# Kernel tuning notes

Hardware: AMD Instinct MI355X
Metric: run time of the kernel (lower is better)

## Reference

```python
import jax, jax.numpy as jnp
import numpy as np

DIM, HEADS, WH, WW, MLAT, MLON = 512, 8, 8, 8, 32, 64
N = WH * WW
B = MLAT * MLON
PER_LAT = (2 * WH - 1) * (2 * WW - 1)  # 225


def _make_rel_idx():
    # Swin 2D relative position index inside one window
    ch, cw = np.arange(WH), np.arange(WW)
    coords = np.stack(np.meshgrid(ch, cw, indexing='ij')).reshape(2, -1)  # (2, N)
    rel = coords[:, :, None] - coords[:, None, :]                          # (2, N, N)
    rel = rel.transpose(1, 2, 0).astype(np.int64)
    rel[..., 0] += WH - 1
    rel[..., 1] += WW - 1
    rel[..., 0] *= 2 * WW - 1
    idx2d = rel.sum(-1)                                                    # (N, N)
    # earth-specific: each lat row i gets its own 225-entry slab; lon diff is 0
    idx = idx2d[None] + np.arange(MLAT)[:, None, None] * PER_LAT           # (Mlat, N, N)
    idx = np.broadcast_to(idx[:, None], (MLAT, MLON, N, N)).reshape(B, N, N)
    return jnp.asarray(idx.astype(np.int32))


def setup_inputs() -> dict:
    key = jax.random.key(0)
    k = jax.random.split(key, 5)
    x = jax.random.normal(k[0], (B, N, DIM), dtype=jnp.float32)
    w_qkv = jax.random.normal(k[1], (3 * DIM, DIM), dtype=jnp.float32) * 0.02
    b_qkv = jnp.zeros((3 * DIM,), dtype=jnp.float32)
    w_proj = jax.random.normal(k[2], (DIM, DIM), dtype=jnp.float32) * 0.02
    b_proj = jnp.zeros((DIM,), dtype=jnp.float32)
    bias_table = jax.random.normal(k[3], (MLAT * PER_LAT, HEADS), dtype=jnp.float32) * 0.02
    return {
        'x': x, 'w_qkv': w_qkv, 'b_qkv': b_qkv,
        'w_proj': w_proj, 'b_proj': b_proj,
        'bias_table': bias_table, 'rel_idx': _make_rel_idx(),
    }


def reference(x, w_qkv, b_qkv, w_proj, b_proj, bias_table, rel_idx):
    Bn, Nn, C = x.shape
    D = C // HEADS
    qkv = (x @ w_qkv.T + b_qkv).reshape(Bn, Nn, 3, HEADS, D)
    q = jnp.transpose(qkv[:, :, 0], (0, 2, 1, 3))  # (B, H, N, D)
    k = jnp.transpose(qkv[:, :, 1], (0, 2, 1, 3))
    v = jnp.transpose(qkv[:, :, 2], (0, 2, 1, 3))
    # gather learned earth bias: (B, N, N, H) -> (B, H, N, N)
    bias = jnp.transpose(bias_table[rel_idx], (0, 3, 1, 2))
    scale = D ** -0.5  # SDPA default scale (qk_scale is None)
    attn = jax.nn.softmax(jnp.einsum('bhnd,bhmd->bhnm', q, k) * scale + bias, axis=-1)
    out = jnp.einsum('bhnm,bhmd->bhnd', attn, v)
    out = jnp.transpose(out, (0, 2, 1, 3)).reshape(Bn, Nn, C)
    return out @ w_proj.T + b_proj
```

## Files before the change

### kernel.cpp

```cpp
#include <hip/hip_runtime.h>
#include <stdint.h>

typedef __attribute__((ext_vector_type(8))) short short8;
typedef __attribute__((ext_vector_type(4))) short short4v;
typedef __attribute__((ext_vector_type(4))) float float4v;

__device__ __forceinline__ short f2bf(float f) {
  uint32_t u = __builtin_bit_cast(uint32_t, f);
  u += 0x7FFFu + ((u >> 16) & 1u);
  return (short)(u >> 16);
}

__device__ __forceinline__ void gl_lds16(const short* g, short* l) {
  __builtin_amdgcn_global_load_lds(
      (const __attribute__((address_space(1))) unsigned int*)g,
      (__attribute__((address_space(3))) unsigned int*)l, 16, 0, 0);
}


__global__ void prep_weights(const float* __restrict__ wq, const float* __restrict__ wp,
                             short* __restrict__ wq_b, short* __restrict__ wp_b) {
  int i = blockIdx.x * blockDim.x + threadIdx.x;
  int stride = gridDim.x * blockDim.x;
  for (int j = i; j < 786432 / 4; j += stride) {
    float4 v = ((const float4*)wq)[j];
    short4v t = {f2bf(v.x), f2bf(v.y), f2bf(v.z), f2bf(v.w)};
    ((short4v*)wq_b)[j] = t;
  }
  for (int j = i; j < 262144 / 4; j += stride) {
    float4 v = ((const float4*)wp)[j];
    short4v t = {f2bf(v.x), f2bf(v.y), f2bf(v.z), f2bf(v.w)};
    ((short4v*)wp_b)[j] = t;
  }
}

__global__ __launch_bounds__(1024, 4)
void qkv_attn(const float* __restrict__ x, const short* __restrict__ wq,
              const float* __restrict__ bqkv, const float* __restrict__ btab,
              short* __restrict__ attn) {
  __shared__ short Xs[64 * 512];
  __shared__ short Qs[4][64 * 64];
  __shared__ short Ks[4][64 * 64];
  __shared__ short Vt[4][64 * 64];

  const int b    = blockIdx.x;
  const int tid  = threadIdx.x;
  const int lane = tid & 63;
  const int w    = tid >> 6;
  const int l16  = lane & 15;
  const int quad = lane >> 4;
  const int lat  = b >> 6;
  const int r    = l16 & 7;
  const int offE = ((quad ^ (r & 3)) << 3) | ((r >> 2) << 5);
  const int offO = offE ^ 32;

  const float* xw = x + (size_t)b * (64 * 512);
  for (int c = tid; c < 64 * 128; c += 1024) {
    int n = c >> 7, kc = c & 127;
    float4 v = *(const float4*)(xw + n * 512 + kc * 4);
    short4v t = {f2bf(v.x), f2bf(v.y), f2bf(v.z), f2bf(v.w)};
    *(short4v*)&Xs[n * 512 + ((kc * 4) ^ ((n & 7) << 3))] = t;
  }
  __syncthreads();

  const int g  = w >> 2;
  const int st = w & 3;

#pragma unroll 1
  for (int h0 = 0; h0 < 8; h0 += 4) {
    {
      const int hq = h0 + g;
      const int hk = h0 + (g ^ 1);
      const short* Aq = wq + (size_t)((hq * 64 + st * 16 + l16) * 512) + quad * 8;
      const short* Ak = wq + (size_t)((512 + hk * 64 + st * 16 + l16) * 512) + quad * 8;
      const short* Av = wq + (size_t)((1024 + hq * 64 + st * 16 + l16) * 512) + quad * 8;
      const short* xE = &Xs[l16 * 512 + offE];
      const short* xO = &Xs[l16 * 512 + offO];

      float4v aQ[4] = {}, aK[4] = {}, aV[4] = {};
#pragma unroll
      for (int j = 0; j < 16; ++j) {
        const short* xb = (j & 1) ? xO : xE;
        const int xoff = (j >> 1) * 64;
        short8 wqf = *(const short8*)(Aq + j * 32);
        short8 wkf = *(const short8*)(Ak + j * 32);
        short8 wvf = *(const short8*)(Av + j * 32);
        short8 x0 = *(const short8*)(xb + xoff);
        short8 x1 = *(const short8*)(xb + 8192 + xoff);
        short8 x2 = *(const short8*)(xb + 16384 + xoff);
        short8 x3 = *(const short8*)(xb + 24576 + xoff);
        aQ[0] = __builtin_amdgcn_mfma_f32_16x16x32_bf16(wqf, x0, aQ[0], 0, 0, 0);
        aQ[1] = __builtin_amdgcn_mfma_f32_16x16x32_bf16(wqf, x1, aQ[1], 0, 0, 0);
        aQ[2] = __builtin_amdgcn_mfma_f32_16x16x32_bf16(wqf, x2, aQ[2], 0, 0, 0);
        aQ[3] = __builtin_amdgcn_mfma_f32_16x16x32_bf16(wqf, x3, aQ[3], 0, 0, 0);
        aK[0] = __builtin_amdgcn_mfma_f32_16x16x32_bf16(wkf, x0, aK[0], 0, 0, 0);
        aK[1] = __builtin_amdgcn_mfma_f32_16x16x32_bf16(wkf, x1, aK[1], 0, 0, 0);
        aK[2] = __builtin_amdgcn_mfma_f32_16x16x32_bf16(wkf, x2, aK[2], 0, 0, 0);
        aK[3] = __builtin_amdgcn_mfma_f32_16x16x32_bf16(wkf, x3, aK[3], 0, 0, 0);
        aV[0] = __builtin_amdgcn_mfma_f32_16x16x32_bf16(x0, wvf, aV[0], 0, 0, 0);
        aV[1] = __builtin_amdgcn_mfma_f32_16x16x32_bf16(x1, wvf, aV[1], 0, 0, 0);
        aV[2] = __builtin_amdgcn_mfma_f32_16x16x32_bf16(x2, wvf, aV[2], 0, 0, 0);
        aV[3] = __builtin_amdgcn_mfma_f32_16x16x32_bf16(x3, wvf, aV[3], 0, 0, 0);
      }

      float bq[4], bk[4];
#pragma unroll
      for (int i = 0; i < 4; ++i) {
        bq[i] = bqkv[hq * 64 + st * 16 + quad * 4 + i];
        bk[i] = bqkv[512 + hk * 64 + st * 16 + quad * 4 + i];
      }
      short* dq = &Qs[g][0];
      short* dk = &Ks[g ^ 1][0];
      const int swqk = (st * 16 + quad * 4) ^ (r << 3);
#pragma unroll
      for (int t = 0; t < 4; ++t) {
        int n = t * 16 + l16;
        short4v pq, pk;
#pragma unroll
        for (int i = 0; i < 4; ++i) {
          pq[i] = f2bf((aQ[t][i] + bq[i]) * 0.125f);
          pk[i] = f2bf(aK[t][i] + bk[i]);
        }
        *(short4v*)&dq[n * 64 + swqk] = pq;
        *(short4v*)&dk[n * 64 + swqk] = pk;
      }
      float bv = bqkv[1024 + hq * 64 + st * 16 + l16];
      const int dv = st * 16 + l16;
#pragma unroll
      for (int t = 0; t < 4; ++t) {
        short4v pv;
#pragma unroll
        for (int i = 0; i < 4; ++i) pv[i] = f2bf(aV[t][i] + bv);
        *(short4v*)&Vt[g][dv * 64 + ((t * 16 + quad * 4) ^ (r << 3))] = pv;
      }
    }
    __syncthreads();

    {
      const int hsel = w >> 2;
      const int h    = h0 + hsel;
      const int n0   = (w & 3) * 16;
      const short* Qb = &Qs[hsel][0];
      const short* Kb = &Ks[hsel][0];
      const short* Vb = &Vt[hsel][0];

      float4v s4[4] = {};
#pragma unroll
      for (int j = 0; j < 2; ++j) {
        const int o = j ? offO : offE;
        short8 a = *(const short8*)&Qb[(n0 + l16) * 64 + o];
#pragma unroll
        for (int t = 0; t < 4; ++t) {
          short8 bf = *(const short8*)&Kb[(t * 16 + l16) * 64 + o];
          s4[t] = __builtin_amdgcn_mfma_f32_16x16x32_bf16(a, bf, s4[t], 0, 0, 0);
        }
      }
#pragma unroll
      for (int t = 0; t < 4; ++t) {
        int m = t * 16 + l16;
#pragma unroll
        for (int i = 0; i < 4; ++i) {
          int n = n0 + quad * 4 + i;
          int idx = ((n >> 3) - (m >> 3) + 7) * 15 + ((n & 7) - (m & 7) + 7) + lat * 225;
          s4[t][i] += btab[idx * 8 + h];
        }
      }
      float p[4][4];
#pragma unroll
      for (int i = 0; i < 4; ++i) {
        float mx = fmaxf(fmaxf(s4[0][i], s4[1][i]), fmaxf(s4[2][i], s4[3][i]));
        mx = fmaxf(mx, __shfl_xor(mx, 1));
        mx = fmaxf(mx, __shfl_xor(mx, 2));
        mx = fmaxf(mx, __shfl_xor(mx, 4));
        mx = fmaxf(mx, __shfl_xor(mx, 8));
        float e0 = __expf(s4[0][i] - mx), e1 = __expf(s4[1][i] - mx);
        float e2 = __expf(s4[2][i] - mx), e3 = __expf(s4[3][i] - mx);
        float sm = e0 + e1 + e2 + e3;
        sm += __shfl_xor(sm, 1);
        sm += __shfl_xor(sm, 2);
        sm += __shfl_xor(sm, 4);
        sm += __shfl_xor(sm, 8);
        float inv = 1.0f / sm;
        p[0][i] = e0 * inv; p[1][i] = e1 * inv; p[2][i] = e2 * inv; p[3][i] = e3 * inv;
      }
      short* Pw = &Qs[hsel][0];
#pragma unroll
      for (int t = 0; t < 4; ++t)
#pragma unroll
        for (int i = 0; i < 4; ++i) {
          int row = n0 + quad * 4 + i;
          Pw[row * 64 + ((t * 16 + l16) ^ ((row & 7) << 3))] = f2bf(p[t][i]);
        }

      float4v o4[4] = {};
#pragma unroll
      for (int j = 0; j < 2; ++j) {
        const int o = j ? offO : offE;
        short8 a = *(const short8*)&Qb[(n0 + l16) * 64 + o];
#pragma unroll
        for (int t = 0; t < 4; ++t) {
          short8 bf = *(const short8*)&Vb[(t * 16 + l16) * 64 + o];
          o4[t] = __builtin_amdgcn_mfma_f32_16x16x32_bf16(a, bf, o4[t], 0, 0, 0);
        }
      }
      short* ob = attn + (size_t)b * (64 * 512);
#pragma unroll
      for (int t = 0; t < 4; ++t)
#pragma unroll
        for (int i = 0; i < 4; ++i)
          ob[(n0 + quad * 4 + i) * 512 + h * 64 + t * 16 + l16] = f2bf(o4[t][i]);
    }
    __syncthreads();
  }
}

__device__ __forceinline__ void stage_tile(const short* __restrict__ ga,
                                           const short* __restrict__ gb,
                                           short* lA, short* lB,
                                           int w, int srow, int scol) {
#pragma unroll
  for (int j = 0; j < 2; ++j) {
    int c = w * 2 + j;
    gl_lds16(ga + (size_t)(c * 8 + srow) * 512 + scol, &lA[c * 512]);
    gl_lds16(gb + (size_t)(c * 8 + srow) * 512 + scol, &lB[c * 512]);
  }
}

__device__ __forceinline__ void compute_tile(const short* As_, const short* Bs_,
                                             float4v (&acc)[2][4],
                                             int wm, int wn, int l16,
                                             int offE, int offO) {
#pragma unroll
  for (int ks = 0; ks < 2; ++ks) {
    const int o = ks ? offO : offE;
    short8 a[2], bf[4];
#pragma unroll
    for (int ti = 0; ti < 2; ++ti)
      a[ti] = *(const short8*)&As_[(wm * 32 + ti * 16 + l16) * 64 + o];
#pragma unroll
    for (int tj = 0; tj < 4; ++tj)
      bf[tj] = *(const short8*)&Bs_[(wn * 64 + tj * 16 + l16) * 64 + o];
#pragma unroll
    for (int ti = 0; ti < 2; ++ti)
#pragma unroll
      for (int tj = 0; tj < 4; ++tj)
        acc[ti][tj] = __builtin_amdgcn_mfma_f32_16x16x32_bf16(a[ti], bf[tj], acc[ti][tj], 0, 0, 0);
  }
}

__global__ __launch_bounds__(512, 4)
void proj_gemm(const short* __restrict__ attn, const short* __restrict__ wp,
               const float* __restrict__ bproj, float* __restrict__ out) {
  __shared__ short As0[128 * 64];
  __shared__ short As1[128 * 64];
  __shared__ short Bs0[128 * 64];
  __shared__ short Bs1[128 * 64];

  const int orig = blockIdx.x;
  const int wg   = (orig & 7) * 512 + (orig >> 3);
  const int n0   = (wg & 3) * 128;
  const int m0   = (wg >> 2) * 128;

  const int tid  = threadIdx.x;
  const int lane = tid & 63;
  const int w    = tid >> 6;
  const int l16  = lane & 15;
  const int quad = lane >> 4;
  const int wm   = w >> 1, wn = w & 1;
  const int r    = l16 & 7;
  const int offE = ((quad ^ (r & 3)) << 3) | ((r >> 2) << 5);
  const int offO = offE ^ 32;

  const int srow = lane >> 3;
  const int scol = ((lane & 7) ^ srow) * 8;

  const short* gA = attn + (size_t)m0 * 512;
  const short* gB = wp + (size_t)n0 * 512;

  float4v acc[2][4] = {};

  stage_tile(gA, gB, As0, Bs0, w, srow, scol);
  __syncthreads();
#pragma unroll
  for (int kt = 0; kt < 8; kt += 2) {
    if (kt + 1 < 8) stage_tile(gA + (kt + 1) * 64, gB + (kt + 1) * 64, As1, Bs1, w, srow, scol);
    compute_tile(As0, Bs0, acc, wm, wn, l16, offE, offO);
    __syncthreads();
    if (kt + 2 < 8) stage_tile(gA + (kt + 2) * 64, gB + (kt + 2) * 64, As0, Bs0, w, srow, scol);
    compute_tile(As1, Bs1, acc, wm, wn, l16, offE, offO);
    __syncthreads();
  }

  float bj[4];
#pragma unroll
  for (int tj = 0; tj < 4; ++tj) bj[tj] = bproj[n0 + wn * 64 + tj * 16 + l16];
#pragma unroll
  for (int ti = 0; ti < 2; ++ti)
#pragma unroll
    for (int i = 0; i < 4; ++i) {
      size_t rowoff = (size_t)(m0 + wm * 32 + ti * 16 + quad * 4 + i) * 512;
#pragma unroll
      for (int tj = 0; tj < 4; ++tj)
        out[rowoff + n0 + wn * 64 + tj * 16 + l16] = acc[ti][tj][i] + bj[tj];
    }
}

extern "C" void kernel_launch(void* const* d_in, const int* in_sizes, int n_in,
                              void* d_out, int out_size, void* d_ws, size_t ws_size,
                              hipStream_t stream) {
  const float* x     = (const float*)d_in[0];
  const float* wqkv  = (const float*)d_in[1];
  const float* bqkv  = (const float*)d_in[2];
  const float* wproj = (const float*)d_in[3];
  const float* bproj = (const float*)d_in[4];
  const float* btab  = (const float*)d_in[5];
  float* out = (float*)d_out;

  short* wq_b = (short*)d_ws;
  short* wp_b = wq_b + 786432;
  short* attn = wp_b + 262144;

  prep_weights<<<256, 256, 0, stream>>>(wqkv, wproj, wq_b, wp_b);
  qkv_attn<<<2048, 1024, 0, stream>>>(x, wq_b, bqkv, btab, attn);
  proj_gemm<<<4096, 512, 0, stream>>>(attn, wp_b, bproj, out);
}
```

Before: 1.069 ms.

## Make attention and projection kernels persistent over multiple windows with weight prefetch

The fused QKV-attention kernel now processes four windows per block (512 blocks instead of 2048), and the projection GEMM processes four M tiles per block (1024 blocks instead of 4096). Bias loads are hoisted out of the GEMM tile loop. The QKV weight fragments are software-pipelined through a three-deep register ring so global loads are issued two steps ahead of the MFMAs. The intent is to cut block launch and prologue overhead and hide weight-load latency. The cost is fewer blocks, which may underfill the GPU or leave a tail imbalance, plus a serial per-window X staging step with no overlap.

```diff
diff --git a/kernel.cpp b/kernel.cpp
--- a/kernel.cpp
+++ b/kernel.cpp
@@ -43,174 +43,187 @@
   __shared__ short Ks[4][64 * 64];
   __shared__ short Vt[4][64 * 64];
 
-  const int b    = blockIdx.x;
+  const int blk  = blockIdx.x;
   const int tid  = threadIdx.x;
   const int lane = tid & 63;
   const int w    = tid >> 6;
   const int l16  = lane & 15;
   const int quad = lane >> 4;
-  const int lat  = b >> 6;
   const int r    = l16 & 7;
   const int offE = ((quad ^ (r & 3)) << 3) | ((r >> 2) << 5);
   const int offO = offE ^ 32;
 
-  const float* xw = x + (size_t)b * (64 * 512);
-  for (int c = tid; c < 64 * 128; c += 1024) {
-    int n = c >> 7, kc = c & 127;
-    float4 v = *(const float4*)(xw + n * 512 + kc * 4);
-    short4v t = {f2bf(v.x), f2bf(v.y), f2bf(v.z), f2bf(v.w)};
-    *(short4v*)&Xs[n * 512 + ((kc * 4) ^ ((n & 7) << 3))] = t;
-  }
-  __syncthreads();
-
   const int g  = w >> 2;
   const int st = w & 3;
 
 #pragma unroll 1
-  for (int h0 = 0; h0 < 8; h0 += 4) {
-    {
-      const int hq = h0 + g;
-      const int hk = h0 + (g ^ 1);
-      const short* Aq = wq + (size_t)((hq * 64 + st * 16 + l16) * 512) + quad * 8;
-      const short* Ak = wq + (size_t)((512 + hk * 64 + st * 16 + l16) * 512) + quad * 8;
-      const short* Av = wq + (size_t)((1024 + hq * 64 + st * 16 + l16) * 512) + quad * 8;
-      const short* xE = &Xs[l16 * 512 + offE];
-      const short* xO = &Xs[l16 * 512 + offO];
-
-      float4v aQ[4] = {}, aK[4] = {}, aV[4] = {};
-#pragma unroll
-      for (int j = 0; j < 16; ++j) {
-        const short* xb = (j & 1) ? xO : xE;
-        const int xoff = (j >> 1) * 64;
-        short8 wqf = *(const short8*)(Aq + j * 32);
-        short8 wkf = *(const short8*)(Ak + j * 32);
-        short8 wvf = *(const short8*)(Av + j * 32);
-        short8 x0 = *(const short8*)(xb + xoff);
-        short8 x1 = *(const short8*)(xb + 8192 + xoff);
-        short8 x2 = *(const short8*)(xb + 16384 + xoff);
-        short8 x3 = *(const short8*)(xb + 24576 + xoff);
-        aQ[0] = __builtin_amdgcn_mfma_f32_16x16x32_bf16(wqf, x0, aQ[0], 0, 0, 0);
-        aQ[1] = __builtin_amdgcn_mfma_f32_16x16x32_bf16(wqf, x1, aQ[1], 0, 0, 0);
-        aQ[2] = __builtin_amdgcn_mfma_f32_16x16x32_bf16(wqf, x2, aQ[2], 0, 0, 0);
-        aQ[3] = __builtin_amdgcn_mfma_f32_16x16x32_bf16(wqf, x3, aQ[3], 0, 0, 0);
-        aK[0] = __builtin_amdgcn_mfma_f32_16x16x32_bf16(wkf, x0, aK[0], 0, 0, 0);
-        aK[1] = __builtin_amdgcn_mfma_f32_16x16x32_bf16(wkf, x1, aK[1], 0, 0, 0);
-        aK[2] = __builtin_amdgcn_mfma_f32_16x16x32_bf16(wkf, x2, aK[2], 0, 0, 0);
-        aK[3] = __builtin_amdgcn_mfma_f32_16x16x32_bf16(wkf, x3, aK[3], 0, 0, 0);
-        aV[0] = __builtin_amdgcn_mfma_f32_16x16x32_bf16(x0, wvf, aV[0], 0, 0, 0);
-        aV[1] = __builtin_amdgcn_mfma_f32_16x16x32_bf16(x1, wvf, aV[1], 0, 0, 0);
-        aV[2] = __builtin_amdgcn_mfma_f32_16x16x32_bf16(x2, wvf, aV[2], 0, 0, 0);
-        aV[3] = __builtin_amdgcn_mfma_f32_16x16x32_bf16(x3, wvf, aV[3], 0, 0, 0);
-      }
-
-      float bq[4], bk[4];
-#pragma unroll
-      for (int i = 0; i < 4; ++i) {
-        bq[i] = bqkv[hq * 64 + st * 16 + quad * 4 + i];
-        bk[i] = bqkv[512 + hk * 64 + st * 16 + quad * 4 + i];
-      }
-      short* dq = &Qs[g][0];
-      short* dk = &Ks[g ^ 1][0];
-      const int swqk = (st * 16 + quad * 4) ^ (r << 3);
-#pragma unroll
-      for (int t = 0; t < 4; ++t) {
-        int n = t * 16 + l16;
-        short4v pq, pk;
-#pragma unroll
-        for (int i = 0; i < 4; ++i) {
-          pq[i] = f2bf((aQ[t][i] + bq[i]) * 0.125f);
-          pk[i] = f2bf(aK[t][i] + bk[i]);
-        }
-        *(short4v*)&dq[n * 64 + swqk] = pq;
-        *(short4v*)&dk[n * 64 + swqk] = pk;
-      }
-      float bv = bqkv[1024 + hq * 64 + st * 16 + l16];
-      const int dv = st * 16 + l16;
-#pragma unroll
-      for (int t = 0; t < 4; ++t) {
-        short4v pv;
-#pragma unroll
-        for (int i = 0; i < 4; ++i) pv[i] = f2bf(aV[t][i] + bv);
-        *(short4v*)&Vt[g][dv * 64 + ((t * 16 + quad * 4) ^ (r << 3))] = pv;
-      }
+  for (int vi = 0; vi < 4; ++vi) {
+    const int b   = blk * 4 + vi;
+    const int lat = b >> 6;
+
+    const float* xw = x + (size_t)b * (64 * 512);
+    for (int c = tid; c < 64 * 128; c += 1024) {
+      int n = c >> 7, kc = c & 127;
+      float4 v = *(const float4*)(xw + n * 512 + kc * 4);
+      short4v t = {f2bf(v.x), f2bf(v.y), f2bf(v.z), f2bf(v.w)};
+      *(short4v*)&Xs[n * 512 + ((kc * 4) ^ ((n & 7) << 3))] = t;
     }
     __syncthreads();
 
-    {
-      const int hsel = w >> 2;
-      const int h    = h0 + hsel;
-      const int n0   = (w & 3) * 16;
-      const short* Qb = &Qs[hsel][0];
-      const short* Kb = &Ks[hsel][0];
-      const short* Vb = &Vt[hsel][0];
-
-      float4v s4[4] = {};
-#pragma unroll
-      for (int j = 0; j < 2; ++j) {
-        const int o = j ? offO : offE;
-        short8 a = *(const short8*)&Qb[(n0 + l16) * 64 + o];
+#pragma unroll 1
+    for (int h0 = 0; h0 < 8; h0 += 4) {
+      {
+        const int hq = h0 + g;
+        const int hk = h0 + (g ^ 1);
+        const short* Aq = wq + (size_t)((hq * 64 + st * 16 + l16) * 512) + quad * 8;
+        const short* Ak = wq + (size_t)((512 + hk * 64 + st * 16 + l16) * 512) + quad * 8;
+        const short* Av = wq + (size_t)((1024 + hq * 64 + st * 16 + l16) * 512) + quad * 8;
+        const short* xE = &Xs[l16 * 512 + offE];
+        const short* xO = &Xs[l16 * 512 + offO];
+
+        short8 wqp[3], wkp[3], wvp[3];
+        wqp[0] = *(const short8*)(Aq);      wqp[1] = *(const short8*)(Aq + 32);
+        wkp[0] = *(const short8*)(Ak);      wkp[1] = *(const short8*)(Ak + 32);
+        wvp[0] = *(const short8*)(Av);      wvp[1] = *(const short8*)(Av + 32);
+
+        float4v aQ[4] = {}, aK[4] = {}, aV[4] = {};
+#pragma unroll
+        for (int j = 0; j < 16; ++j) {
+          if (j + 2 < 16) {
+            wqp[(j + 2) % 3] = *(const short8*)(Aq + (j + 2) * 32);
+            wkp[(j + 2) % 3] = *(const short8*)(Ak + (j + 2) * 32);
+            wvp[(j + 2) % 3] = *(const short8*)(Av + (j + 2) * 32);
+          }
+          const short* xb = (j & 1) ? xO : xE;
+          const int xoff = (j >> 1) * 64;
+          short8 x0 = *(const short8*)(xb + xoff);
+          short8 x1 = *(const short8*)(xb + 8192 + xoff);
+          short8 x2 = *(const short8*)(xb + 16384 + xoff);
+          short8 x3 = *(const short8*)(xb + 24576 + xoff);
+          short8 Wq = wqp[j % 3], Wk = wkp[j % 3], Wv = wvp[j % 3];
+          aQ[0] = __builtin_amdgcn_mfma_f32_16x16x32_bf16(Wq, x0, aQ[0], 0, 0, 0);
+          aQ[1] = __builtin_amdgcn_mfma_f32_16x16x32_bf16(Wq, x1, aQ[1], 0, 0, 0);
+          aQ[2] = __builtin_amdgcn_mfma_f32_16x16x32_bf16(Wq, x2, aQ[2], 0, 0, 0);
+          aQ[3] = __builtin_amdgcn_mfma_f32_16x16x32_bf16(Wq, x3, aQ[3], 0, 0, 0);
+          aK[0] = __builtin_amdgcn_mfma_f32_16x16x32_bf16(Wk, x0, aK[0], 0, 0, 0);
+          aK[1] = __builtin_amdgcn_mfma_f32_16x16x32_bf16(Wk, x1, aK[1], 0, 0, 0);
+          aK[2] = __builtin_amdgcn_mfma_f32_16x16x32_bf16(Wk, x2, aK[2], 0, 0, 0);
+          aK[3] = __builtin_amdgcn_mfma_f32_16x16x32_bf16(Wk, x3, aK[3], 0, 0, 0);
+          aV[0] = __builtin_amdgcn_mfma_f32_16x16x32_bf16(x0, Wv, aV[0], 0, 0, 0);
+          aV[1] = __builtin_amdgcn_mfma_f32_16x16x32_bf16(x1, Wv, aV[1], 0, 0, 0);
+          aV[2] = __builtin_amdgcn_mfma_f32_16x16x32_bf16(x2, Wv, aV[2], 0, 0, 0);
+          aV[3] = __builtin_amdgcn_mfma_f32_16x16x32_bf16(x3, Wv, aV[3], 0, 0, 0);
+        }
+
+        float bq[4], bk[4];
+#pragma unroll
+        for (int i = 0; i < 4; ++i) {
+          bq[i] = bqkv[hq * 64 + st * 16 + quad * 4 + i];
+          bk[i] = bqkv[512 + hk * 64 + st * 16 + quad * 4 + i];
+        }
+        short* dq = &Qs[g][0];
+        short* dk = &Ks[g ^ 1][0];
+        const int swqk = (st * 16 + quad * 4) ^ (r << 3);
 #pragma unroll
         for (int t = 0; t < 4; ++t) {
-          short8 bf = *(const short8*)&Kb[(t * 16 + l16) * 64 + o];
-          s4[t] = __builtin_amdgcn_mfma_f32_16x16x32_bf16(a, bf, s4[t], 0, 0, 0);
+          int n = t * 16 + l16;
+          short4v pq, pk;
+#pragma unroll
+          for (int i = 0; i < 4; ++i) {
+            pq[i] = f2bf((aQ[t][i] + bq[i]) * 0.125f);
+            pk[i] = f2bf(aK[t][i] + bk[i]);
+          }
+          *(short4v*)&dq[n * 64 + swqk] = pq;
+          *(short4v*)&dk[n * 64 + swqk] = pk;
+        }
+        float bv = bqkv[1024 + hq * 64 + st * 16 + l16];
+        const int dv = st * 16 + l16;
+#pragma unroll
+        for (int t = 0; t < 4; ++t) {
+          short4v pv;
+#pragma unroll
+          for (int i = 0; i < 4; ++i) pv[i] = f2bf(aV[t][i] + bv);
+          *(short4v*)&Vt[g][dv * 64 + ((t * 16 + quad * 4) ^ (r << 3))] = pv;
         }
       }
-#pragma unroll
-      for (int t = 0; t < 4; ++t) {
-        int m = t * 16 + l16;
+      __syncthreads();
+
+      {
+        const int hsel = w >> 2;
+        const int h    = h0 + hsel;
+        const int n0   = (w & 3) * 16;
+        const short* Qb = &Qs[hsel][0];
+        const short* Kb = &Ks[hsel][0];
+        const short* Vb = &Vt[hsel][0];
+
+        float4v s4[4] = {};
+#pragma unroll
+        for (int j = 0; j < 2; ++j) {
+          const int o = j ? offO : offE;
+          short8 a = *(const short8*)&Qb[(n0 + l16) * 64 + o];
+#pragma unroll
+          for (int t = 0; t < 4; ++t) {
+            short8 bf = *(const short8*)&Kb[(t * 16 + l16) * 64 + o];
+            s4[t] = __builtin_amdgcn_mfma_f32_16x16x32_bf16(a, bf, s4[t], 0, 0, 0);
+          }
+        }
+#pragma unroll
+        for (int t = 0; t < 4; ++t) {
+          int m = t * 16 + l16;
+#pragma unroll
+          for (int i = 0; i < 4; ++i) {
+            int n = n0 + quad * 4 + i;
+            int idx = ((n >> 3) - (m >> 3) + 7) * 15 + ((n & 7) - (m & 7) + 7) + lat * 225;
+            s4[t][i] += btab[idx * 8 + h];
+          }
+        }
+        float p[4][4];
 #pragma unroll
         for (int i = 0; i < 4; ++i) {
-          int n = n0 + quad * 4 + i;
-          int idx = ((n >> 3) - (m >> 3) + 7) * 15 + ((n & 7) - (m & 7) + 7) + lat * 225;
-          s4[t][i] += btab[idx * 8 + h];
-        }
+          float mx = fmaxf(fmaxf(s4[0][i], s4[1][i]), fmaxf(s4[2][i], s4[3][i]));
+          mx = fmaxf(mx, __shfl_xor(mx, 1));
+          mx = fmaxf(mx, __shfl_xor(mx, 2));
+          mx = fmaxf(mx, __shfl_xor(mx, 4));
+          mx = fmaxf(mx, __shfl_xor(mx, 8));
+          float e0 = __expf(s4[0][i] - mx), e1 = __expf(s4[1][i] - mx);
+          float e2 = __expf(s4[2][i] - mx), e3 = __expf(s4[3][i] - mx);
+          float sm = e0 + e1 + e2 + e3;
+          sm += __shfl_xor(sm, 1);
+          sm += __shfl_xor(sm, 2);
+          sm += __shfl_xor(sm, 4);
+          sm += __shfl_xor(sm, 8);
+          float inv = 1.0f / sm;
+          p[0][i] = e0 * inv; p[1][i] = e1 * inv; p[2][i] = e2 * inv; p[3][i] = e3 * inv;
+        }
+        short* Pw = &Qs[hsel][0];
+#pragma unroll
+        for (int t = 0; t < 4; ++t)
+#pragma unroll
+          for (int i = 0; i < 4; ++i) {
+            int row = n0 + quad * 4 + i;
+            Pw[row * 64 + ((t * 16 + l16) ^ ((row & 7) << 3))] = f2bf(p[t][i]);
+          }
+
+        float4v o4[4] = {};
+#pragma unroll
+        for (int j = 0; j < 2; ++j) {
+          const int o = j ? offO : offE;
+          short8 a = *(const short8*)&Qb[(n0 + l16) * 64 + o];
+#pragma unroll
+          for (int t = 0; t < 4; ++t) {
+            short8 bf = *(const short8*)&Vb[(t * 16 + l16) * 64 + o];
+            o4[t] = __builtin_amdgcn_mfma_f32_16x16x32_bf16(a, bf, o4[t], 0, 0, 0);
+          }
+        }
+        short* ob = attn + (size_t)b * (64 * 512);
+#pragma unroll
+        for (int t = 0; t < 4; ++t)
+#pragma unroll
+          for (int i = 0; i < 4; ++i)
+            ob[(n0 + quad * 4 + i) * 512 + h * 64 + t * 16 + l16] = f2bf(o4[t][i]);
       }
-      float p[4][4];
-#pragma unroll
-      for (int i = 0; i < 4; ++i) {
-        float mx = fmaxf(fmaxf(s4[0][i], s4[1][i]), fmaxf(s4[2][i], s4[3][i]));
-        mx = fmaxf(mx, __shfl_xor(mx, 1));
-        mx = fmaxf(mx, __shfl_xor(mx, 2));
-        mx = fmaxf(mx, __shfl_xor(mx, 4));
-        mx = fmaxf(mx, __shfl_xor(mx, 8));
-        float e0 = __expf(s4[0][i] - mx), e1 = __expf(s4[1][i] - mx);
-        float e2 = __expf(s4[2][i] - mx), e3 = __expf(s4[3][i] - mx);
-        float sm = e0 + e1 + e2 + e3;
-        sm += __shfl_xor(sm, 1);
-        sm += __shfl_xor(sm, 2);
-        sm += __shfl_xor(sm, 4);
-        sm += __shfl_xor(sm, 8);
-        float inv = 1.0f / sm;
-        p[0][i] = e0 * inv; p[1][i] = e1 * inv; p[2][i] = e2 * inv; p[3][i] = e3 * inv;
-      }
-      short* Pw = &Qs[hsel][0];
-#pragma unroll
-      for (int t = 0; t < 4; ++t)
-#pragma unroll
-        for (int i = 0; i < 4; ++i) {
-          int row = n0 + quad * 4 + i;
-          Pw[row * 64 + ((t * 16 + l16) ^ ((row & 7) << 3))] = f2bf(p[t][i]);
-        }
-
-      float4v o4[4] = {};
-#pragma unroll
-      for (int j = 0; j < 2; ++j) {
-        const int o = j ? offO : offE;
-        short8 a = *(const short8*)&Qb[(n0 + l16) * 64 + o];
-#pragma unroll
-        for (int t = 0; t < 4; ++t) {
-          short8 bf = *(const short8*)&Vb[(t * 16 + l16) * 64 + o];
-          o4[t] = __builtin_amdgcn_mfma_f32_16x16x32_bf16(a, bf, o4[t], 0, 0, 0);
-        }
-      }
-      short* ob = attn + (size_t)b * (64 * 512);
-#pragma unroll
-      for (int t = 0; t < 4; ++t)
-#pragma unroll
-        for (int i = 0; i < 4; ++i)
-          ob[(n0 + quad * 4 + i) * 512 + h * 64 + t * 16 + l16] = f2bf(o4[t][i]);
+      __syncthreads();
     }
-    __syncthreads();
   }
 }
 
@@ -257,9 +270,9 @@
   __shared__ short Bs1[128 * 64];
 
   const int orig = blockIdx.x;
-  const int wg   = (orig & 7) * 512 + (orig >> 3);
+  const int wg   = (orig & 7) * 128 + (orig >> 3);
   const int n0   = (wg & 3) * 128;
-  const int m0   = (wg >> 2) * 128;
+  const int mp   = wg >> 2;
 
   const int tid  = threadIdx.x;
   const int lane = tid & 63;
@@ -274,35 +287,41 @@
   const int srow = lane >> 3;
   const int scol = ((lane & 7) ^ srow) * 8;
 
-  const short* gA = attn + (size_t)m0 * 512;
   const short* gB = wp + (size_t)n0 * 512;
 
-  float4v acc[2][4] = {};
-
-  stage_tile(gA, gB, As0, Bs0, w, srow, scol);
-  __syncthreads();
-#pragma unroll
-  for (int kt = 0; kt < 8; kt += 2) {
-    if (kt + 1 < 8) stage_tile(gA + (kt + 1) * 64, gB + (kt + 1) * 64, As1, Bs1, w, srow, scol);
-    compute_tile(As0, Bs0, acc, wm, wn, l16, offE, offO);
+  float bj[4];
+#pragma unroll
+  for (int tj = 0; tj < 4; ++tj) bj[tj] = bproj[n0 + wn * 64 + tj * 16 + l16];
+
+#pragma unroll 1
+  for (int it = 0; it < 4; ++it) {
+    const int m0 = mp * 512 + it * 128;
+    const short* gA = attn + (size_t)m0 * 512;
+
+    float4v acc[2][4] = {};
+
+    stage_tile(gA, gB, As0, Bs0, w, srow, scol);
     __syncthreads();
-    if (kt + 2 < 8) stage_tile(gA + (kt + 2) * 64, gB + (kt + 2) * 64, As0, Bs0, w, srow, scol);
-    compute_tile(As1, Bs1, acc, wm, wn, l16, offE, offO);
-    __syncthreads();
-  }
-
-  float bj[4];
-#pragma unroll
-  for (int tj = 0; tj < 4; ++tj) bj[tj] = bproj[n0 + wn * 64 + tj * 16 + l16];
-#pragma unroll
-  for (int ti = 0; ti < 2; ++ti)
-#pragma unroll
-    for (int i = 0; i < 4; ++i) {
-      size_t rowoff = (size_t)(m0 + wm * 32 + ti * 16 + quad * 4 + i) * 512;
-#pragma unroll
-      for (int tj = 0; tj < 4; ++tj)
-        out[rowoff + n0 + wn * 64 + tj * 16 + l16] = acc[ti][tj][i] + bj[tj];
+#pragma unroll
+    for (int kt = 0; kt < 8; kt += 2) {
+      if (kt + 1 < 8) stage_tile(gA + (kt + 1) * 64, gB + (kt + 1) * 64, As1, Bs1, w, srow, scol);
+      compute_tile(As0, Bs0, acc, wm, wn, l16, offE, offO);
+      __syncthreads();
+      if (kt + 2 < 8) stage_tile(gA + (kt + 2) * 64, gB + (kt + 2) * 64, As0, Bs0, w, srow, scol);
+      compute_tile(As1, Bs1, acc, wm, wn, l16, offE, offO);
+      __syncthreads();
     }
+
+#pragma unroll
+    for (int ti = 0; ti < 2; ++ti)
+#pragma unroll
+      for (int i = 0; i < 4; ++i) {
+        size_t rowoff = (size_t)(m0 + wm * 32 + ti * 16 + quad * 4 + i) * 512;
+#pragma unroll
+        for (int tj = 0; tj < 4; ++tj)
+          out[rowoff + n0 + wn * 64 + tj * 16 + l16] = acc[ti][tj][i] + bj[tj];
+      }
+  }
 }
 
 extern "C" void kernel_launch(void* const* d_in, const int* in_sizes, int n_in,
@@ -321,6 +340,6 @@
   short* attn = wp_b + 262144;
 
   prep_weights<<<256, 256, 0, stream>>>(wqkv, wproj, wq_b, wp_b);
-  qkv_attn<<<2048, 1024, 0, stream>>>(x, wq_b, bqkv, btab, attn);
-  proj_gemm<<<4096, 512, 0, stream>>>(attn, wp_b, bproj, out);
-}
+  qkv_attn<<<512, 1024, 0, stream>>>(x, wq_b, bqkv, btab, attn);
+  proj_gemm<<<1024, 512, 0, stream>>>(attn, wp_b, bproj, out);
+}
```

Measured after the change: 1.045 ms. -2.2%, faster.
